# Optimization experiments

Hardware: AMD Instinct MI355X
Metric: run time of the kernel (lower is better)

The kernel has to match this reference:

```python
import jax, jax.numpy as jnp
import numpy as np

N_HEADS = 16
HEAD_SIZE = 64
N_EMBD = N_HEADS * HEAD_SIZE  # 1024
B, T = 4, 2048


def setup_inputs() -> dict:
    key = jax.random.key(0)
    kx, kq, kk, kv, kp = jax.random.split(key, 5)
    s = 1.0 / np.sqrt(N_EMBD)
    return {
        "x": jax.random.normal(kx, (B, T, N_EMBD), dtype=jnp.float32),
        "Wq": jax.random.normal(kq, (N_EMBD, N_HEADS * HEAD_SIZE), dtype=jnp.float32) * s,
        "Wk": jax.random.normal(kk, (N_EMBD, N_HEADS * HEAD_SIZE), dtype=jnp.float32) * s,
        "Wv": jax.random.normal(kv, (N_EMBD, N_HEADS * HEAD_SIZE), dtype=jnp.float32) * s,
        "Wp": jax.random.normal(kp, (N_HEADS * HEAD_SIZE, N_EMBD), dtype=jnp.float32) * s,
    }


def reference(x, Wq, Wk, Wv, Wp):
    Bb, Tt, C = x.shape
    H, hs = N_HEADS, HEAD_SIZE
    # QKV projections (no bias), split heads: (B, H, T, hs)
    q = (x @ Wq).reshape(Bb, Tt, H, hs).transpose(0, 2, 1, 3)
    k = (x @ Wk).reshape(Bb, Tt, H, hs).transpose(0, 2, 1, 3)
    v = (x @ Wv).reshape(Bb, Tt, H, hs).transpose(0, 2, 1, 3)
    scores = jnp.einsum("bhqd,bhkd->bhqk", q, k) / np.sqrt(hs).astype(np.float32)
    causal = jnp.tril(jnp.ones((Tt, Tt), dtype=bool))
    scores = jnp.where(causal, scores, -jnp.inf)
    attn = jax.nn.softmax(scores, axis=-1)  # dropout p=0 -> identity
    o = jnp.einsum("bhqk,bhkd->bhqd", attn, v)  # (B, H, T, hs)
    # Faithfully replicate torch's view/transpose/view sequence:
    o = o.reshape(Bb, Tt, H * hs)          # raw reshape of (B,H,T,hs) buffer
    o = jnp.swapaxes(o, 1, 2)               # (B, H*hs, T)
    o = o.reshape(Bb, Tt, H * hs)           # contiguous().view
    return o @ Wp
```

## Files before the change

kernel.cpp:

```cpp
#include <hip/hip_runtime.h>

typedef unsigned short ush;
typedef unsigned int u32;
typedef __attribute__((ext_vector_type(4))) float f32x4;
typedef __attribute__((ext_vector_type(8))) short short8;
typedef __attribute__((ext_vector_type(8))) ush ushx8;
typedef __attribute__((ext_vector_type(4))) ush ushx4;

#define GAS __attribute__((address_space(1)))
#define LAS __attribute__((address_space(3)))

__device__ __forceinline__ void gl_lds16(const void* g, void* l) {
  __builtin_amdgcn_global_load_lds((const GAS void*)g, (LAS void*)l, 16, 0, 0);
}

__device__ __forceinline__ ush f2bf(float f) {
  union { float f; unsigned int u; } x; x.f = f;
  unsigned int r = x.u + 0x7fffu + ((x.u >> 16) & 1u);
  return (ush)(r >> 16);
}
__device__ __forceinline__ u32 fbits(float f) {
  union { float f; u32 u; } x; x.f = f; return x.u;
}

#define NEG_BIG (-1.0e4f)
#define SCL 0.18033688f

__global__ __launch_bounds__(256) void k_prep(
    const float* __restrict__ X, const float* __restrict__ W0,
    const float* __restrict__ W1, const float* __restrict__ W2,
    const float* __restrict__ W3, ush* __restrict__ Xb, ush* __restrict__ Wt) {
  __shared__ ush Ts[64][72];
  const int bx = blockIdx.x;
  if (bx < 4096) {
    int idx = bx * 256 + threadIdx.x;
    int base = idx * 8;
    f32x4 a = *(const f32x4*)(X + base);
    f32x4 b = *(const f32x4*)(X + base + 4);
    ushx8 o;
#pragma unroll
    for (int q = 0; q < 4; ++q) { o[q] = f2bf(a[q]); o[4 + q] = f2bf(b[q]); }
    *(ushx8*)(Xb + base) = o;
    return;
  }
  const int bid = bx - 4096;
  const int z = bid >> 8;
  const int k0 = (bid & 15) * 64, n0 = ((bid >> 4) & 15) * 64;
  const float* W = (z == 0) ? W0 : (z == 1) ? W1 : (z == 2) ? W2 : W3;
  ush* Ot = Wt + (size_t)z * 1048576;
  const int rr = threadIdx.x >> 4, cc = threadIdx.x & 15;
#pragma unroll
  for (int i = 0; i < 4; ++i) {
    int row = i * 16 + rr;
    f32x4 v = *(const f32x4*)(W + (size_t)(k0 + row) * 1024 + n0 + cc * 4);
#pragma unroll
    for (int q = 0; q < 4; ++q) Ts[row][cc * 4 + q] = f2bf(v[q]);
  }
  __syncthreads();
#pragma unroll
  for (int i = 0; i < 4; ++i) {
    int n = i * 16 + rr;
    ushx4 o;
#pragma unroll
    for (int q = 0; q < 4; ++q) o[q] = Ts[cc * 4 + q][n];
    *(ushx4*)(Ot + (size_t)(n0 + n) * 1024 + k0 + cc * 4) = o;
  }
}

__global__ __launch_bounds__(512, 2) void k_gemm_qkv(
    const ush* __restrict__ X, const ush* __restrict__ Wt,
    ush* __restrict__ QKV, ush* __restrict__ Vtg) {
  __shared__ __align__(16) ush As_[2][16384];
  __shared__ __align__(16) ush Bs_[2][8192];
  const int tid = threadIdx.x;
  const int w = tid >> 6, l = tid & 63, lr = l & 15, lg = l >> 4;
  const int wm = w >> 2, wn = w & 3;
  const int mt = blockIdx.x, nt = blockIdx.y;
  const int which = nt >> 3, n0 = (nt & 7) * 128;
  const ush* Ag = X + (size_t)mt * 256 * 1024;
  const ush* Bg = Wt + (size_t)which * 1048576 + (size_t)n0 * 1024;
  int aoff[4], boff[2];
#pragma unroll
  for (int it = 0; it < 4; ++it) {
    int ch = it * 512 + tid, row = ch >> 3, g = ch & 7;
    aoff[it] = row * 1024 + ((g ^ (row & 7)) << 3);
  }
#pragma unroll
  for (int it = 0; it < 2; ++it) {
    int ch = it * 512 + tid, row = ch >> 3, g = ch & 7;
    boff[it] = row * 1024 + ((g ^ (row & 7)) << 3);
  }
  f32x4 acc[8][2] = {};

  auto issueS = [&](int kt, int buf) {
    const ush* Asrc = Ag + kt * 64;
    const ush* Bsrc = Bg + kt * 64;
#pragma unroll
    for (int it = 0; it < 4; ++it)
      gl_lds16(Asrc + aoff[it], &As_[buf][((size_t)it * 512 + tid) * 8]);
#pragma unroll
    for (int it = 0; it < 2; ++it)
      gl_lds16(Bsrc + boff[it], &Bs_[buf][((size_t)it * 512 + tid) * 8]);
  };

  issueS(0, 0);
  for (int t = 0; t < 16; ++t) {
    if (t < 15) {
      issueS(t + 1, (t + 1) & 1);
      asm volatile("s_waitcnt vmcnt(6)" ::: "memory");
    } else {
      asm volatile("s_waitcnt vmcnt(0)" ::: "memory");
    }
    __syncthreads();
    const ush* Ab = As_[t & 1];
    const ush* Bb = Bs_[t & 1];
    short8 fb[2][2];
#pragma unroll
    for (int ni = 0; ni < 2; ++ni)
#pragma unroll
      for (int kk = 0; kk < 2; ++kk) {
        int row = wn * 32 + ni * 16 + lr;
        fb[ni][kk] = *(const short8*)(Bb + row * 64 + (((kk * 4 + lg) ^ (row & 7)) << 3));
      }
#pragma unroll
    for (int qm = 0; qm < 4; ++qm) {
      short8 fa[2][2];
#pragma unroll
      for (int m2 = 0; m2 < 2; ++m2)
#pragma unroll
        for (int kk = 0; kk < 2; ++kk) {
          int row = wm * 128 + (qm * 2 + m2) * 16 + lr;
          fa[m2][kk] = *(const short8*)(Ab + row * 64 + (((kk * 4 + lg) ^ (row & 7)) << 3));
        }
      __builtin_amdgcn_s_setprio(1);
#pragma unroll
      for (int m2 = 0; m2 < 2; ++m2)
#pragma unroll
        for (int ni = 0; ni < 2; ++ni)
#pragma unroll
          for (int kk = 0; kk < 2; ++kk)
            acc[qm * 2 + m2][ni] = __builtin_amdgcn_mfma_f32_16x16x32_bf16(
                fa[m2][kk], fb[ni][kk], acc[qm * 2 + m2][ni], 0, 0, 0);
      __builtin_amdgcn_s_setprio(0);
    }
    __syncthreads();
  }
  ush* Ct = &As_[0][0];
#pragma unroll
  for (int mi = 0; mi < 8; ++mi)
#pragma unroll
    for (int ni = 0; ni < 2; ++ni)
#pragma unroll
      for (int j = 0; j < 4; ++j)
        Ct[(wm * 128 + mi * 16 + lg * 4 + j) * 128 + wn * 32 + ni * 16 + lr] =
            f2bf(acc[mi][ni][j]);
  __syncthreads();
  const int m0 = mt * 256, b = m0 >> 11, t0 = m0 & 2047, h0 = n0 >> 6;
  if (which == 2) {
    const int cc = tid & 127, rq = tid >> 7;
    const int hsel = cc >> 6, d = cc & 63;
    ush* dst = Vtg + (size_t)(b * 16 + h0 + hsel) * 131072 + (size_t)d * 2048 +
               t0 + rq * 64;
#pragma unroll
    for (int ch = 0; ch < 8; ++ch) {
      ushx8 v;
#pragma unroll
      for (int k = 0; k < 8; ++k) v[k] = Ct[(rq * 64 + ch * 8 + k) * 128 + cc];
      *(ushx8*)(dst + ch * 8) = v;
    }
  } else {
    ush* Om = QKV + (size_t)which * 8388608;
#pragma unroll
    for (int it = 0; it < 8; ++it) {
      int c = it * 512 + tid;
      int hsel = c >> 11;
      int cc = c & 2047;
      int r = cc >> 3;
      int c8 = (cc & 7) * 8;
      ushx8 v = *(const ushx8*)(Ct + r * 128 + hsel * 64 + c8);
      *(ushx8*)(Om + ((size_t)(b * 16 + h0 + hsel) * 2048 + t0 + r) * 64 + c8) = v;
    }
  }
}

__global__ __launch_bounds__(256) void k_attn(
    const ush* __restrict__ Q, const ush* __restrict__ K,
    const ush* __restrict__ Vg, ush* __restrict__ O) {
  __shared__ __align__(16) ush Ks[2][4096];
  __shared__ __align__(16) ush Vs[2][4096];
  __shared__ __align__(16) ush Pl[8][1024];
  const int lid = blockIdx.x + 16 * blockIdx.y;
  const int qta = (lid >> 3) & 15;
  const int bh  = ((lid >> 7) << 3) | (lid & 7);
  const int qtb = 31 - qta;
  const size_t hb = (size_t)bh * (2048 * 64);
  const ush* Qh = Q + hb;
  const ush* Kh = K + hb;
  const ush* Vh = Vg + hb;
  const int tid = threadIdx.x, w = tid >> 6, l = tid & 63, lr = l & 15, lg = l >> 4;
  const int q0a = qta * 64 + w * 16, q0b = qtb * 64 + w * 16;

  short8 qfa[2], qfb[2];
#pragma unroll
  for (int s = 0; s < 2; ++s) {
    qfa[s] = *(const short8*)(Qh + (size_t)(q0a + lr) * 64 + s * 32 + lg * 8);
    qfb[s] = *(const short8*)(Qh + (size_t)(q0b + lr) * 64 + s * 32 + lg * 8);
  }
  f32x4 acca[4] = {}, accb[4] = {};
  float la[4] = {0.f, 0.f, 0.f, 0.f}, lb[4] = {0.f, 0.f, 0.f, 0.f};

  int koff[2], voff[2];
#pragma unroll
  for (int it = 0; it < 2; ++it) {
    int ch = it * 256 + tid;
    int r = ch >> 3, g = ch & 7;
    koff[it] = r * 64 + ((g ^ (r & 7)) << 3);
    int keyv = ((r & 7) + (r >> 3)) & 7;
    voff[it] = r * 2048 + ((g ^ keyv) << 3);
  }
  auto issueStage = [&](int c, int buf) {
#pragma unroll
    for (int it = 0; it < 2; ++it) {
      int ch = it * 256 + tid;
      gl_lds16(Kh + (size_t)c * 4096 + koff[it], &Ks[buf][ch * 8]);
      gl_lds16(Vh + c * 64 + voff[it], &Vs[buf][ch * 8]);
    }
  };

  auto ctile = [&](const ush* Kc, const ush* Vc, const short8* qf,
                   f32x4* acc, float* lrow, bool diag, ush* PlW) {
    f32x4 sf[4] = {};
#pragma unroll
    for (int s = 0; s < 2; ++s)
#pragma unroll
      for (int f = 0; f < 4; ++f) {
        int kv = f * 16 + lr;
        short8 kf = *(const short8*)(Kc + kv * 64 + (((s * 4 + lg) ^ (kv & 7)) << 3));
        sf[f] = __builtin_amdgcn_mfma_f32_16x16x32_bf16(qf[s], kf, sf[f], 0, 0, 0);
      }
#pragma unroll
    for (int f = 0; f < 4; ++f)
#pragma unroll
      for (int j = 0; j < 4; ++j) {
        float vv = sf[f][j] * SCL;
        if (diag && (f * 16 + lr) > (w * 16 + lg * 4 + j)) vv = NEG_BIG;
        sf[f][j] = __builtin_amdgcn_exp2f(vv);
      }
#pragma unroll
    for (int j = 0; j < 4; ++j)
      lrow[j] += (sf[0][j] + sf[1][j]) + (sf[2][j] + sf[3][j]);
#pragma unroll
    for (int f = 0; f < 4; ++f)
#pragma unroll
      for (int j = 0; j < 4; ++j) {
        int q = lg * 4 + j;
        PlW[q * 64 + ((f * 16 + lr) ^ ((q & 7) << 3))] = (ush)(fbits(sf[f][j]) >> 16);
      }
#pragma unroll
    for (int s = 0; s < 2; ++s) {
      short8 pf = *(const short8*)(PlW + lr * 64 + (((s * 4 + lg) ^ (lr & 7)) << 3));
#pragma unroll
      for (int db = 0; db < 4; ++db) {
        int dv = db * 16 + lr;
        int keyv = ((dv & 7) + (dv >> 3)) & 7;
        short8 vf = *(const short8*)(Vc + dv * 64 + (((s * 4 + lg) ^ keyv) << 3));
        acc[db] = __builtin_amdgcn_mfma_f32_16x16x32_bf16(pf, vf, acc[db], 0, 0, 0);
      }
    }
  };

  issueStage(0, 0);
  int cur = 0;
  for (int c = 0; c <= qtb; ++c) {
    asm volatile("s_waitcnt vmcnt(0)" ::: "memory");
    __syncthreads();
    if (c < qtb) issueStage(c + 1, cur ^ 1);
    const ush* Kc = Ks[cur];
    const ush* Vc = Vs[cur];
    if (c <= qta) ctile(Kc, Vc, qfa, acca, la, c == qta, Pl[w]);
    ctile(Kc, Vc, qfb, accb, lb, c == qtb, Pl[4 + w]);
    cur ^= 1;
  }

#pragma unroll
  for (int msk = 1; msk <= 8; msk <<= 1)
#pragma unroll
    for (int j = 0; j < 4; ++j) {
      la[j] += __shfl_xor(la[j], msk);
      lb[j] += __shfl_xor(lb[j], msk);
    }
  float ia[4], ib[4];
#pragma unroll
  for (int j = 0; j < 4; ++j) {
    ia[j] = __builtin_amdgcn_rcpf(la[j]);
    ib[j] = __builtin_amdgcn_rcpf(lb[j]);
  }
  ush* Oh = O + hb;
#pragma unroll
  for (int db = 0; db < 4; ++db)
#pragma unroll
    for (int j = 0; j < 4; ++j) {
      Oh[(size_t)(q0a + lg * 4 + j) * 64 + db * 16 + lr] = f2bf(acca[db][j] * ia[j]);
      Oh[(size_t)(q0b + lg * 4 + j) * 64 + db * 16 + lr] = f2bf(accb[db][j] * ib[j]);
    }
}

__global__ __launch_bounds__(256) void k_gather(const ush* __restrict__ Ob, ush* __restrict__ Mb) {
  __shared__ ush Ls[2][128][68];
  const int jh = blockIdx.x, tau = blockIdx.y, b = blockIdx.z;
  const int tid = threadIdx.x;
#pragma unroll
  for (int it = 0; it < 8; ++it) {
    int c = it * 256 + tid;
    int r = c >> 3, d8 = (c & 7) * 8;
    int esel = r >> 7, jlow = r & 127;
    ushx8 v = *(const ushx8*)(Ob +
        ((size_t)(b * 16 + jh + esel * 8) * 2048 + jlow * 16 + tau) * 64 + d8);
    *(ushx8*)(&Ls[esel][jlow][d8]) = v;
  }
  __syncthreads();
  const int wv = tid >> 6, l = tid & 63;
  const int e = wv >> 1, jhalf = wv & 1, d = l;
  ush* Mrow = Mb + (size_t)b * 2097152 +
              (size_t)(128 * tau + 2 * d + e) * 1024 + jh * 128 + jhalf * 64;
#pragma unroll
  for (int ch = 0; ch < 8; ++ch) {
    ushx8 v;
#pragma unroll
    for (int k = 0; k < 8; ++k) v[k] = Ls[e][jhalf * 64 + ch * 8 + k][d];
    *(ushx8*)(Mrow + ch * 8) = v;
  }
}

__global__ __launch_bounds__(512, 2) void k_gemm_out(
    const ush* __restrict__ A, const ush* __restrict__ Bt, float* __restrict__ Out) {
  __shared__ __align__(16) ush As_[2][16384];
  __shared__ __align__(16) ush Bs_[2][8192];
  const int tid = threadIdx.x;
  const int w = tid >> 6, l = tid & 63, lr = l & 15, lg = l >> 4;
  const int wm = w >> 2, wn = w & 3;
  const int mt = blockIdx.x, nt = blockIdx.y;
  const int n0 = nt * 128;
  const ush* Ag = A + (size_t)mt * 256 * 1024;
  const ush* Bg = Bt + (size_t)n0 * 1024;
  int aoff[4], boff[2];
#pragma unroll
  for (int it = 0; it < 4; ++it) {
    int ch = it * 512 + tid, row = ch >> 3, g = ch & 7;
    aoff[it] = row * 1024 + ((g ^ (row & 7)) << 3);
  }
#pragma unroll
  for (int it = 0; it < 2; ++it) {
    int ch = it * 512 + tid, row = ch >> 3, g = ch & 7;
    boff[it] = row * 1024 + ((g ^ (row & 7)) << 3);
  }
  f32x4 acc[8][2] = {};

  auto issueS = [&](int kt, int buf) {
    const ush* Asrc = Ag + kt * 64;
    const ush* Bsrc = Bg + kt * 64;
#pragma unroll
    for (int it = 0; it < 4; ++it)
      gl_lds16(Asrc + aoff[it], &As_[buf][((size_t)it * 512 + tid) * 8]);
#pragma unroll
    for (int it = 0; it < 2; ++it)
      gl_lds16(Bsrc + boff[it], &Bs_[buf][((size_t)it * 512 + tid) * 8]);
  };

  issueS(0, 0);
  for (int t = 0; t < 16; ++t) {
    if (t < 15) {
      issueS(t + 1, (t + 1) & 1);
      asm volatile("s_waitcnt vmcnt(6)" ::: "memory");
    } else {
      asm volatile("s_waitcnt vmcnt(0)" ::: "memory");
    }
    __syncthreads();
    const ush* Ab = As_[t & 1];
    const ush* Bb = Bs_[t & 1];
    short8 fb[2][2];
#pragma unroll
    for (int ni = 0; ni < 2; ++ni)
#pragma unroll
      for (int kk = 0; kk < 2; ++kk) {
        int row = wn * 32 + ni * 16 + lr;
        fb[ni][kk] = *(const short8*)(Bb + row * 64 + (((kk * 4 + lg) ^ (row & 7)) << 3));
      }
#pragma unroll
    for (int qm = 0; qm < 4; ++qm) {
      short8 fa[2][2];
#pragma unroll
      for (int m2 = 0; m2 < 2; ++m2)
#pragma unroll
        for (int kk = 0; kk < 2; ++kk) {
          int row = wm * 128 + (qm * 2 + m2) * 16 + lr;
          fa[m2][kk] = *(const short8*)(Ab + row * 64 + (((kk * 4 + lg) ^ (row & 7)) << 3));
        }
      __builtin_amdgcn_s_setprio(1);
#pragma unroll
      for (int m2 = 0; m2 < 2; ++m2)
#pragma unroll
        for (int ni = 0; ni < 2; ++ni)
#pragma unroll
          for (int kk = 0; kk < 2; ++kk)
            acc[qm * 2 + m2][ni] = __builtin_amdgcn_mfma_f32_16x16x32_bf16(
                fa[m2][kk], fb[ni][kk], acc[qm * 2 + m2][ni], 0, 0, 0);
      __builtin_amdgcn_s_setprio(0);
    }
    __syncthreads();
  }
  const int m0 = mt * 256;
#pragma unroll
  for (int mi = 0; mi < 8; ++mi)
#pragma unroll
    for (int ni = 0; ni < 2; ++ni)
#pragma unroll
      for (int j = 0; j < 4; ++j)
        Out[(size_t)(m0 + wm * 128 + mi * 16 + lg * 4 + j) * 1024 +
            n0 + wn * 32 + ni * 16 + lr] = acc[mi][ni][j];
}

extern "C" void kernel_launch(void* const* d_in, const int* in_sizes, int n_in,
                              void* d_out, int out_size, void* d_ws, size_t ws_size,
                              hipStream_t stream) {
  const float* x  = (const float*)d_in[0];
  const float* wq = (const float*)d_in[1];
  const float* wk = (const float*)d_in[2];
  const float* wv = (const float*)d_in[3];
  const float* wp = (const float*)d_in[4];
  float* out = (float*)d_out;
  char* ws = (char*)d_ws;
  ush* xb  = (ush*)ws;
  ush* wt  = (ush*)(ws + 16777216);
  ush* qkv = (ush*)(ws + 25165824);
  ush* vtg = (ush*)(ws + 75497472);
  ush* ob  = qkv;
  ush* mb  = xb;

  k_prep<<<dim3(5120), 256, 0, stream>>>(x, wq, wk, wv, wp, xb, wt);
  k_gemm_qkv<<<dim3(32, 24), 512, 0, stream>>>(xb, wt, qkv, vtg);
  k_attn<<<dim3(16, 64), 256, 0, stream>>>(qkv, qkv + 8388608, vtg, ob);
  k_gather<<<dim3(8, 16, 4), 256, 0, stream>>>(ob, mb);
  k_gemm_out<<<dim3(32, 8), 512, 0, stream>>>(mb, wt + 3145728, out);
}
```

Measured before the change: 206.7 us.

## Use three-stage K=32 LDS pipeline with single barrier in projection GEMMs

Both the QKV and output-projection GEMMs move from a double-buffered K=64 tile to a triple-buffered K=32 tile. The prefetch for stage t+2 is issued after the barrier, which removes the trailing __syncthreads per iteration. A new XOR swizzle key is used for the 4-chunk rows. LDS use falls from 96KB to about 72KB per block, which could help occupancy. In exchange the loop runs twice as many iterations with half the MFMA work each, so fixed per-iteration overhead goes up.

Result: faster. 195.3 us (-5.5%).

```diff
diff --git a/kernel.cpp b/kernel.cpp
--- a/kernel.cpp
+++ b/kernel.cpp
@@ -25,6 +25,8 @@
 
 #define NEG_BIG (-1.0e4f)
 #define SCL 0.18033688f
+
+__device__ __forceinline__ int kkey(int row) { return ((row & 3) + (row >> 2)) & 3; }
 
 __global__ __launch_bounds__(256) void k_prep(
     const float* __restrict__ X, const float* __restrict__ W0,
@@ -70,8 +72,7 @@
 __global__ __launch_bounds__(512, 2) void k_gemm_qkv(
     const ush* __restrict__ X, const ush* __restrict__ Wt,
     ush* __restrict__ QKV, ush* __restrict__ Vtg) {
-  __shared__ __align__(16) ush As_[2][16384];
-  __shared__ __align__(16) ush Bs_[2][8192];
+  __shared__ __align__(16) ush sm[36864];
   const int tid = threadIdx.x;
   const int w = tid >> 6, l = tid & 63, lr = l & 15, lg = l >> 4;
   const int wm = w >> 2, wn = w & 3;
@@ -79,73 +80,69 @@
   const int which = nt >> 3, n0 = (nt & 7) * 128;
   const ush* Ag = X + (size_t)mt * 256 * 1024;
   const ush* Bg = Wt + (size_t)which * 1048576 + (size_t)n0 * 1024;
-  int aoff[4], boff[2];
-#pragma unroll
-  for (int it = 0; it < 4; ++it) {
-    int ch = it * 512 + tid, row = ch >> 3, g = ch & 7;
-    aoff[it] = row * 1024 + ((g ^ (row & 7)) << 3);
-  }
-#pragma unroll
-  for (int it = 0; it < 2; ++it) {
-    int ch = it * 512 + tid, row = ch >> 3, g = ch & 7;
-    boff[it] = row * 1024 + ((g ^ (row & 7)) << 3);
+  int aoff[2], boff;
+  {
+#pragma unroll
+    for (int it = 0; it < 2; ++it) {
+      int ch = it * 512 + tid, row = ch >> 2, g = ch & 3;
+      aoff[it] = row * 1024 + ((g ^ kkey(row)) << 3);
+    }
+    int row = tid >> 2, g = tid & 3;
+    boff = row * 1024 + ((g ^ kkey(row)) << 3);
   }
   f32x4 acc[8][2] = {};
 
-  auto issueS = [&](int kt, int buf) {
-    const ush* Asrc = Ag + kt * 64;
-    const ush* Bsrc = Bg + kt * 64;
-#pragma unroll
-    for (int it = 0; it < 4; ++it)
-      gl_lds16(Asrc + aoff[it], &As_[buf][((size_t)it * 512 + tid) * 8]);
+  auto issueS = [&](int kt, int st) {
+    const ush* Asrc = Ag + kt * 32;
+    const ush* Bsrc = Bg + kt * 32;
+    ush* base = sm + st * 12288;
 #pragma unroll
     for (int it = 0; it < 2; ++it)
-      gl_lds16(Bsrc + boff[it], &Bs_[buf][((size_t)it * 512 + tid) * 8]);
+      gl_lds16(Asrc + aoff[it], base + ((size_t)it * 512 + tid) * 8);
+    gl_lds16(Bsrc + boff, base + 8192 + (size_t)tid * 8);
   };
 
   issueS(0, 0);
-  for (int t = 0; t < 16; ++t) {
-    if (t < 15) {
-      issueS(t + 1, (t + 1) & 1);
-      asm volatile("s_waitcnt vmcnt(6)" ::: "memory");
+  issueS(1, 1);
+  int st = 0, st2 = 2;
+  for (int t = 0; t < 32; ++t) {
+    if (t < 31) {
+      asm volatile("s_waitcnt vmcnt(3)" ::: "memory");
     } else {
       asm volatile("s_waitcnt vmcnt(0)" ::: "memory");
     }
     __syncthreads();
-    const ush* Ab = As_[t & 1];
-    const ush* Bb = Bs_[t & 1];
-    short8 fb[2][2];
-#pragma unroll
-    for (int ni = 0; ni < 2; ++ni)
-#pragma unroll
-      for (int kk = 0; kk < 2; ++kk) {
-        int row = wn * 32 + ni * 16 + lr;
-        fb[ni][kk] = *(const short8*)(Bb + row * 64 + (((kk * 4 + lg) ^ (row & 7)) << 3));
-      }
+    if (t + 2 < 32) issueS(t + 2, st2);
+    const ush* Ab = sm + st * 12288;
+    const ush* Bb = sm + st * 12288 + 8192;
+    short8 fb[2];
+#pragma unroll
+    for (int ni = 0; ni < 2; ++ni) {
+      int row = wn * 32 + ni * 16 + lr;
+      fb[ni] = *(const short8*)(Bb + row * 32 + ((lg ^ kkey(row)) << 3));
+    }
 #pragma unroll
     for (int qm = 0; qm < 4; ++qm) {
-      short8 fa[2][2];
+      short8 fa[2];
+#pragma unroll
+      for (int m2 = 0; m2 < 2; ++m2) {
+        int row = wm * 128 + (qm * 2 + m2) * 16 + lr;
+        fa[m2] = *(const short8*)(Ab + row * 32 + ((lg ^ kkey(row)) << 3));
+      }
+      __builtin_amdgcn_s_setprio(1);
 #pragma unroll
       for (int m2 = 0; m2 < 2; ++m2)
 #pragma unroll
-        for (int kk = 0; kk < 2; ++kk) {
-          int row = wm * 128 + (qm * 2 + m2) * 16 + lr;
-          fa[m2][kk] = *(const short8*)(Ab + row * 64 + (((kk * 4 + lg) ^ (row & 7)) << 3));
-        }
-      __builtin_amdgcn_s_setprio(1);
-#pragma unroll
-      for (int m2 = 0; m2 < 2; ++m2)
-#pragma unroll
         for (int ni = 0; ni < 2; ++ni)
-#pragma unroll
-          for (int kk = 0; kk < 2; ++kk)
-            acc[qm * 2 + m2][ni] = __builtin_amdgcn_mfma_f32_16x16x32_bf16(
-                fa[m2][kk], fb[ni][kk], acc[qm * 2 + m2][ni], 0, 0, 0);
+          acc[qm * 2 + m2][ni] = __builtin_amdgcn_mfma_f32_16x16x32_bf16(
+              fa[m2], fb[ni], acc[qm * 2 + m2][ni], 0, 0, 0);
       __builtin_amdgcn_s_setprio(0);
     }
-    __syncthreads();
-  }
-  ush* Ct = &As_[0][0];
+    st = (st == 2) ? 0 : st + 1;
+    st2 = (st2 == 2) ? 0 : st2 + 1;
+  }
+  __syncthreads();
+  ush* Ct = sm;
 #pragma unroll
   for (int mi = 0; mi < 8; ++mi)
 #pragma unroll
@@ -334,8 +331,7 @@
 
 __global__ __launch_bounds__(512, 2) void k_gemm_out(
     const ush* __restrict__ A, const ush* __restrict__ Bt, float* __restrict__ Out) {
-  __shared__ __align__(16) ush As_[2][16384];
-  __shared__ __align__(16) ush Bs_[2][8192];
+  __shared__ __align__(16) ush sm[36864];
   const int tid = threadIdx.x;
   const int w = tid >> 6, l = tid & 63, lr = l & 15, lg = l >> 4;
   const int wm = w >> 2, wn = w & 3;
@@ -343,71 +339,66 @@
   const int n0 = nt * 128;
   const ush* Ag = A + (size_t)mt * 256 * 1024;
   const ush* Bg = Bt + (size_t)n0 * 1024;
-  int aoff[4], boff[2];
-#pragma unroll
-  for (int it = 0; it < 4; ++it) {
-    int ch = it * 512 + tid, row = ch >> 3, g = ch & 7;
-    aoff[it] = row * 1024 + ((g ^ (row & 7)) << 3);
-  }
-#pragma unroll
-  for (int it = 0; it < 2; ++it) {
-    int ch = it * 512 + tid, row = ch >> 3, g = ch & 7;
-    boff[it] = row * 1024 + ((g ^ (row & 7)) << 3);
+  int aoff[2], boff;
+  {
+#pragma unroll
+    for (int it = 0; it < 2; ++it) {
+      int ch = it * 512 + tid, row = ch >> 2, g = ch & 3;
+      aoff[it] = row * 1024 + ((g ^ kkey(row)) << 3);
+    }
+    int row = tid >> 2, g = tid & 3;
+    boff = row * 1024 + ((g ^ kkey(row)) << 3);
   }
   f32x4 acc[8][2] = {};
 
-  auto issueS = [&](int kt, int buf) {
-    const ush* Asrc = Ag + kt * 64;
-    const ush* Bsrc = Bg + kt * 64;
-#pragma unroll
-    for (int it = 0; it < 4; ++it)
-      gl_lds16(Asrc + aoff[it], &As_[buf][((size_t)it * 512 + tid) * 8]);
+  auto issueS = [&](int kt, int st) {
+    const ush* Asrc = Ag + kt * 32;
+    const ush* Bsrc = Bg + kt * 32;
+    ush* base = sm + st * 12288;
 #pragma unroll
     for (int it = 0; it < 2; ++it)
-      gl_lds16(Bsrc + boff[it], &Bs_[buf][((size_t)it * 512 + tid) * 8]);
+      gl_lds16(Asrc + aoff[it], base + ((size_t)it * 512 + tid) * 8);
+    gl_lds16(Bsrc + boff, base + 8192 + (size_t)tid * 8);
   };
 
   issueS(0, 0);
-  for (int t = 0; t < 16; ++t) {
-    if (t < 15) {
-      issueS(t + 1, (t + 1) & 1);
-      asm volatile("s_waitcnt vmcnt(6)" ::: "memory");
+  issueS(1, 1);
+  int st = 0, st2 = 2;
+  for (int t = 0; t < 32; ++t) {
+    if (t < 31) {
+      asm volatile("s_waitcnt vmcnt(3)" ::: "memory");
     } else {
       asm volatile("s_waitcnt vmcnt(0)" ::: "memory");
     }
     __syncthreads();
-    const ush* Ab = As_[t & 1];
-    const ush* Bb = Bs_[t & 1];
-    short8 fb[2][2];
-#pragma unroll
-    for (int ni = 0; ni < 2; ++ni)
-#pragma unroll
-      for (int kk = 0; kk < 2; ++kk) {
-        int row = wn * 32 + ni * 16 + lr;
-        fb[ni][kk] = *(const short8*)(Bb + row * 64 + (((kk * 4 + lg) ^ (row & 7)) << 3));
-      }
+    if (t + 2 < 32) issueS(t + 2, st2);
+    const ush* Ab = sm + st * 12288;
+    const ush* Bb = sm + st * 12288 + 8192;
+    short8 fb[2];
+#pragma unroll
+    for (int ni = 0; ni < 2; ++ni) {
+      int row = wn * 32 + ni * 16 + lr;
+      fb[ni] = *(const short8*)(Bb + row * 32 + ((lg ^ kkey(row)) << 3));
+    }
 #pragma unroll
     for (int qm = 0; qm < 4; ++qm) {
-      short8 fa[2][2];
+      short8 fa[2];
+#pragma unroll
+      for (int m2 = 0; m2 < 2; ++m2) {
+        int row = wm * 128 + (qm * 2 + m2) * 16 + lr;
+        fa[m2] = *(const short8*)(Ab + row * 32 + ((lg ^ kkey(row)) << 3));
+      }
+      __builtin_amdgcn_s_setprio(1);
 #pragma unroll
       for (int m2 = 0; m2 < 2; ++m2)
 #pragma unroll
-        for (int kk = 0; kk < 2; ++kk) {
-          int row = wm * 128 + (qm * 2 + m2) * 16 + lr;
-          fa[m2][kk] = *(const short8*)(Ab + row * 64 + (((kk * 4 + lg) ^ (row & 7)) << 3));
-        }
-      __builtin_amdgcn_s_setprio(1);
-#pragma unroll
-      for (int m2 = 0; m2 < 2; ++m2)
-#pragma unroll
         for (int ni = 0; ni < 2; ++ni)
-#pragma unroll
-          for (int kk = 0; kk < 2; ++kk)
-            acc[qm * 2 + m2][ni] = __builtin_amdgcn_mfma_f32_16x16x32_bf16(
-                fa[m2][kk], fb[ni][kk], acc[qm * 2 + m2][ni], 0, 0, 0);
+          acc[qm * 2 + m2][ni] = __builtin_amdgcn_mfma_f32_16x16x32_bf16(
+              fa[m2], fb[ni], acc[qm * 2 + m2][ni], 0, 0, 0);
       __builtin_amdgcn_s_setprio(0);
     }
-    __syncthreads();
+    st = (st == 2) ? 0 : st + 1;
+    st2 = (st2 == 2) ? 0 : st2 + 1;
   }
   const int m0 = mt * 256;
 #pragma unroll
```
